# Optimization experiments

Hardware: AMD Instinct MI355X
Metric: run time of the kernel (lower is better)

## Reference

```python
import jax, jax.numpy as jnp
import numpy as np

N_NODES = 20000
N_EDGES = 320000
D_IN = 512
D_OUT = 512


def setup_inputs() -> dict:
    key = jax.random.key(0)
    k1, k2, k3, k4, k5, k6 = jax.random.split(key, 6)
    stdv = 1.0 / np.sqrt(D_OUT)
    return {
        "h": jax.random.normal(k1, (N_NODES, D_IN), dtype=jnp.float32),
        "weight": jax.random.uniform(k2, (D_IN, D_OUT), dtype=jnp.float32, minval=-stdv, maxval=stdv),
        "bias": jax.random.uniform(k3, (D_OUT,), dtype=jnp.float32, minval=-stdv, maxval=stdv),
        # GCN symmetric normalization term per node (deg^{-1/2}); strictly positive
        "norm": jax.random.uniform(k4, (N_NODES, 1), dtype=jnp.float32, minval=0.05, maxval=1.0),
        "src": jax.random.randint(k5, (N_EDGES,), 0, N_NODES, dtype=jnp.int32),
        "dst": jax.random.randint(k6, (N_EDGES,), 0, N_NODES, dtype=jnp.int32),
    }


def reference(h, weight, bias, norm, src, dst):
    # dropout p=0 -> identity (eval mode)
    # pre-normalize after dense projection: [N, d_out]
    hw = norm * jnp.matmul(h, weight)
    # update_all(copy_u, sum): gather source features, scatter-sum into dst
    msg = hw[src]  # [E, d_out]
    agg = jax.ops.segment_sum(msg, dst, num_segments=N_NODES)  # [N, d_out]
    out = agg * norm + bias
    return jax.nn.relu(out)
```

## Files before the change

### kernel.cpp

```cpp
#include <hip/hip_runtime.h>

#define M_NODES 20000
#define N_EDGES_C 320000
#define DIM 512

typedef __attribute__((ext_vector_type(4))) float f32x4;
typedef __attribute__((ext_vector_type(4))) __bf16 bf16x4;
typedef __attribute__((ext_vector_type(8))) __bf16 bf16x8;

__device__ __forceinline__ void async16(__bf16* lds, const __bf16* g) {
  __builtin_amdgcn_global_load_lds(
      (const __attribute__((address_space(1))) void*)g,
      (__attribute__((address_space(3))) void*)lds, 16, 0, 0);
}

__global__ __launch_bounds__(256) void zero_k(int4* __restrict__ counts4) {
  const int i = blockIdx.x * 256 + threadIdx.x;
  if (i < M_NODES / 4) counts4[i] = int4{0, 0, 0, 0};
}

__global__ __launch_bounds__(256) void pre_k(const float* __restrict__ h,
                                             const float* __restrict__ w,
                                             const float* __restrict__ norm,
                                             const int* __restrict__ dst,
                                             __bf16* __restrict__ hb,
                                             __bf16* __restrict__ wT,
                                             int* __restrict__ counts) {
  const int bid = blockIdx.x;
  const int tid = threadIdx.x;
  const int gtid = bid * 256 + tid;
  const int gsz = gridDim.x * 256;

  for (int i = gtid; i < M_NODES * DIM / 4; i += gsz) {
    const int elem = i * 4;
    const float s = norm[elem >> 9];
    f32x4 v = *(const f32x4*)&h[elem];
    bf16x4 o;
    o.x = (__bf16)(v.x * s);
    o.y = (__bf16)(v.y * s);
    o.z = (__bf16)(v.z * s);
    o.w = (__bf16)(v.w * s);
    *(bf16x4*)&hb[elem] = o;
  }

  if (bid < 256) {
    __shared__ float tile[32][33];
    const int bx = (bid & 15) * 32, by = (bid >> 4) * 32;
    const int tx = tid & 31, ty8 = tid >> 5;
#pragma unroll
    for (int st = 0; st < 4; ++st) {
      const int r = ty8 + st * 8;
      tile[r][tx] = w[(by + r) * DIM + bx + tx];
    }
    __syncthreads();
#pragma unroll
    for (int st = 0; st < 4; ++st) {
      const int r = ty8 + st * 8;
      wT[(bx + r) * DIM + by + tx] = (__bf16)tile[tx][r];
    }
  }

  for (int e = gtid; e < N_EDGES_C; e += gsz) atomicAdd(&counts[dst[e]], 1);
}

__global__ __launch_bounds__(256) void scan_k(int* __restrict__ counts,
                                              int* __restrict__ offsets) {
  __shared__ int wsum2[4];
  const int tid = threadIdx.x;
  const int lane = tid & 63, wid = tid >> 6;
  const int base = tid * 80;
  int s = 0;
  if (tid < 250) {
#pragma unroll
    for (int i = 0; i < 80; i += 4) {
      int4 c = *(const int4*)&counts[base + i];
      s += c.x + c.y + c.z + c.w;
    }
  }
  int x = s;
#pragma unroll
  for (int off = 1; off < 64; off <<= 1) {
    int t = __shfl_up(x, off, 64);
    if (lane >= off) x += t;
  }
  if (lane == 63) wsum2[wid] = x;
  __syncthreads();
  int wbase = 0;
  for (int wI = 0; wI < wid; ++wI) wbase += wsum2[wI];
  int run = wbase + x - s;
  if (tid < 250) {
#pragma unroll
    for (int i = 0; i < 80; i += 4) {
      int4 c = *(const int4*)&counts[base + i];
      int4 o;
      o.x = run;
      o.y = run + c.x;
      o.z = o.y + c.y;
      o.w = o.z + c.z;
      *(int4*)&offsets[base + i] = o;
      *(int4*)&counts[base + i] = o;
      run = o.w + c.w;
    }
  }
  if (tid == 0) {
    int tot = 0;
#pragma unroll
    for (int wI = 0; wI < 4; ++wI) tot += wsum2[wI];
    offsets[M_NODES] = tot;
  }
}

__global__ __launch_bounds__(256) void fill_k(const int* __restrict__ src,
                                              const int* __restrict__ dst,
                                              int* __restrict__ cursor,
                                              int* __restrict__ esrc) {
  int e = blockIdx.x * 256 + threadIdx.x;
  if (e < N_EDGES_C) {
    int p = atomicAdd(&cursor[dst[e]], 1);
    esrc[p] = src[e];
  }
}

__global__ __launch_bounds__(256) void aggregate_k(const __bf16* __restrict__ hb,
                                                   const int* __restrict__ offs,
                                                   const int* __restrict__ esrc,
                                                   __bf16* __restrict__ aggb) {
  const int panel = blockIdx.x & 7;
  const int nb = blockIdx.x >> 3;
  const int wv = threadIdx.x >> 6;
  const int lane = threadIdx.x & 63;
  const int slot = lane >> 3;
  const int cg = lane & 7;
  const int node = nb * 32 + wv * 8 + slot;

  const int beg = offs[node], end = offs[node + 1];
  const size_t pbase = (size_t)panel * 64 + cg * 8;

  float a[8] = {};
  int j = beg;
  while (j + 8 <= end) {
    const int idx = esrc[j + cg];
    int sid[8];
#pragma unroll
    for (int g = 0; g < 8; ++g) sid[g] = __shfl(idx, (lane & 56) + g, 64);
    bf16x8 v[8];
#pragma unroll
    for (int g = 0; g < 8; ++g)
      v[g] = *(const bf16x8*)&hb[(size_t)sid[g] * DIM + pbase];
#pragma unroll
    for (int g = 0; g < 8; ++g)
#pragma unroll
      for (int q = 0; q < 8; ++q) a[q] += (float)v[g][q];
    j += 8;
  }
  for (; j < end; ++j) {
    const int s0 = esrc[j];
    bf16x8 v0 = *(const bf16x8*)&hb[(size_t)s0 * DIM + pbase];
#pragma unroll
    for (int q = 0; q < 8; ++q) a[q] += (float)v0[q];
  }
  bf16x8 o;
#pragma unroll
  for (int q = 0; q < 8; ++q) o[q] = (__bf16)a[q];
  *(bf16x8*)&aggb[(size_t)node * DIM + pbase] = o;
}

__global__ __launch_bounds__(256, 2) void gemm_k(const __bf16* __restrict__ A,
                                                 const __bf16* __restrict__ B,
                                                 const float* __restrict__ bias,
                                                 const float* __restrict__ norm,
                                                 float* __restrict__ C) {
  __shared__ __bf16 As[2][64 * 64];
  __shared__ __bf16 Bs[2][128 * 64];
  const int tid = threadIdx.x;
  const int lane = tid & 63;
  const int wv = tid >> 6;
  const int wr = wv >> 1, wc = wv & 1;
  const int m0 = blockIdx.x * 64;
  const int n0 = blockIdx.y * 128;

  f32x4 acc[2][4] = {};

  const int srow = tid >> 3;
  const int scol = ((tid & 7) ^ (srow & 7)) * 8;

  auto stage = [&](int buf, int kt) {
    const int kb = kt * 64 + scol;
#pragma unroll
    for (int jj = 0; jj < 2; ++jj) {
      const int lrow = jj * 32 + srow;
      int arow = m0 + lrow;
      arow = arow < M_NODES ? arow : (M_NODES - 1);
      async16(&As[buf][lrow * 64 + (tid & 7) * 8], A + (size_t)arow * DIM + kb);
    }
#pragma unroll
    for (int jj = 0; jj < 4; ++jj) {
      const int lrow = jj * 32 + srow;
      async16(&Bs[buf][lrow * 64 + (tid & 7) * 8], B + (size_t)(n0 + lrow) * DIM + kb);
    }
  };

  stage(0, 0);
  __syncthreads();

  int cur = 0;
  for (int kt = 0; kt < DIM / 64; ++kt) {
    if (kt + 1 < DIM / 64) stage(cur ^ 1, kt + 1);
#pragma unroll
    for (int kk = 0; kk < 64; kk += 32) {
      const int c = (kk >> 3) + (lane >> 4);
      bf16x8 af[2], bfr[4];
#pragma unroll
      for (int m = 0; m < 2; ++m) {
        const int r = wr * 32 + m * 16 + (lane & 15);
        af[m] = *(const bf16x8*)&As[cur][r * 64 + ((c ^ (r & 7)) * 8)];
      }
#pragma unroll
      for (int n = 0; n < 4; ++n) {
        const int r = wc * 64 + n * 16 + (lane & 15);
        bfr[n] = *(const bf16x8*)&Bs[cur][r * 64 + ((c ^ (r & 7)) * 8)];
      }
#pragma unroll
      for (int m = 0; m < 2; ++m)
#pragma unroll
        for (int n = 0; n < 4; ++n)
          acc[m][n] = __builtin_amdgcn_mfma_f32_16x16x32_bf16(af[m], bfr[n], acc[m][n], 0, 0, 0);
    }
    __syncthreads();
    cur ^= 1;
  }

#pragma unroll
  for (int m = 0; m < 2; ++m) {
    const int rbase = m0 + wr * 32 + m * 16 + (lane >> 4) * 4;
#pragma unroll
    for (int r = 0; r < 4; ++r) {
      const int row = rbase + r;
      if (row < M_NODES) {
        const float nv = norm[row];
#pragma unroll
        for (int n = 0; n < 4; ++n) {
          const int col = n0 + wc * 64 + n * 16 + (lane & 15);
          float v = acc[m][n][r] * nv + bias[col];
          C[(size_t)row * DIM + col] = v > 0.f ? v : 0.f;
        }
      }
    }
  }
}

#define HB_OFF   0UL
#define AGG_OFF  20480000UL
#define WT_OFF   40960000UL
#define CNT_OFF  41484288UL
#define OFS_OFF  41564288UL
#define ESRC_OFF 41644544UL
#define WS_NEEDED 42924544UL

extern "C" void kernel_launch(void* const* d_in, const int* in_sizes, int n_in,
                              void* d_out, int out_size, void* d_ws, size_t ws_size,
                              hipStream_t stream) {
  const float* h    = (const float*)d_in[0];
  const float* w    = (const float*)d_in[1];
  const float* bias = (const float*)d_in[2];
  const float* norm = (const float*)d_in[3];
  const int*   src  = (const int*)d_in[4];
  const int*   dst  = (const int*)d_in[5];
  float* out = (float*)d_out;

  if (ws_size < WS_NEEDED) return;

  char* ws = (char*)d_ws;
  __bf16* hb      = (__bf16*)(ws + HB_OFF);
  __bf16* aggb    = (__bf16*)(ws + AGG_OFF);
  __bf16* wT      = (__bf16*)(ws + WT_OFF);
  int*    counts  = (int*)(ws + CNT_OFF);
  int*    offsets = (int*)(ws + OFS_OFF);
  int*    esrc    = (int*)(ws + ESRC_OFF);

  zero_k<<<20, 256, 0, stream>>>((int4*)counts);
  pre_k<<<2048, 256, 0, stream>>>(h, w, norm, dst, hb, wT, counts);
  scan_k<<<1, 256, 0, stream>>>(counts, offsets);
  fill_k<<<1250, 256, 0, stream>>>(src, dst, counts, esrc);
  aggregate_k<<<5000, 256, 0, stream>>>(hb, offsets, esrc, aggb);
  gemm_k<<<dim3(313, 4), 256, 0, stream>>>(aggb, wT, bias, norm, out);
}
```

Before: 119.7 us.

## Fold scan into pre kernel via last-block detection; triple-buffer GEMM pipeline

The separate single-block scan launch is removed. The last block to finish pre_k, detected with an atomic arrival counter, now performs the prefix scan, which saves one kernel launch and its gap. The GEMM moves from double to triple-buffered LDS staging, with explicit vmcnt waits and one barrier per k-step, so loads run two stages ahead. This raises LDS use per block, which may reduce occupancy, and it relies on correct fence and atomic ordering for the counts.

```diff
diff --git a/kernel.cpp b/kernel.cpp
--- a/kernel.cpp
+++ b/kernel.cpp
@@ -14,9 +14,11 @@
       (__attribute__((address_space(3))) void*)lds, 16, 0, 0);
 }
 
-__global__ __launch_bounds__(256) void zero_k(int4* __restrict__ counts4) {
+__global__ __launch_bounds__(256) void zero_k(int4* __restrict__ counts4,
+                                              int* __restrict__ arrive) {
   const int i = blockIdx.x * 256 + threadIdx.x;
   if (i < M_NODES / 4) counts4[i] = int4{0, 0, 0, 0};
+  if (i == 0) *arrive = 0;
 }
 
 __global__ __launch_bounds__(256) void pre_k(const float* __restrict__ h,
@@ -25,7 +27,9 @@
                                              const int* __restrict__ dst,
                                              __bf16* __restrict__ hb,
                                              __bf16* __restrict__ wT,
-                                             int* __restrict__ counts) {
+                                             int* __restrict__ counts,
+                                             int* __restrict__ offsets,
+                                             int* __restrict__ arrive) {
   const int bid = blockIdx.x;
   const int tid = threadIdx.x;
   const int gtid = bid * 256 + tid;
@@ -61,52 +65,53 @@
   }
 
   for (int e = gtid; e < N_EDGES_C; e += gsz) atomicAdd(&counts[dst[e]], 1);
-}
-
-__global__ __launch_bounds__(256) void scan_k(int* __restrict__ counts,
-                                              int* __restrict__ offsets) {
+
   __shared__ int wsum2[4];
-  const int tid = threadIdx.x;
-  const int lane = tid & 63, wid = tid >> 6;
-  const int base = tid * 80;
-  int s = 0;
-  if (tid < 250) {
-#pragma unroll
-    for (int i = 0; i < 80; i += 4) {
-      int4 c = *(const int4*)&counts[base + i];
-      s += c.x + c.y + c.z + c.w;
-    }
-  }
-  int x = s;
-#pragma unroll
-  for (int off = 1; off < 64; off <<= 1) {
-    int t = __shfl_up(x, off, 64);
-    if (lane >= off) x += t;
-  }
-  if (lane == 63) wsum2[wid] = x;
+  __shared__ int s_last;
+  __threadfence();
   __syncthreads();
-  int wbase = 0;
-  for (int wI = 0; wI < wid; ++wI) wbase += wsum2[wI];
-  int run = wbase + x - s;
-  if (tid < 250) {
-#pragma unroll
-    for (int i = 0; i < 80; i += 4) {
-      int4 c = *(const int4*)&counts[base + i];
-      int4 o;
-      o.x = run;
-      o.y = run + c.x;
-      o.z = o.y + c.y;
-      o.w = o.z + c.z;
-      *(int4*)&offsets[base + i] = o;
-      *(int4*)&counts[base + i] = o;
-      run = o.w + c.w;
-    }
-  }
   if (tid == 0) {
-    int tot = 0;
-#pragma unroll
-    for (int wI = 0; wI < 4; ++wI) tot += wsum2[wI];
-    offsets[M_NODES] = tot;
+    int prev = atomicAdd(arrive, 1);
+    s_last = (prev == (int)gridDim.x - 1) ? 1 : 0;
+  }
+  __syncthreads();
+  if (s_last) {
+    const int lane = tid & 63, wid = tid >> 6;
+    const int base = tid * 80;
+    int s = 0;
+    if (tid < 250) {
+#pragma unroll
+      for (int i = 0; i < 80; ++i)
+        s += __hip_atomic_load(&counts[base + i], __ATOMIC_RELAXED,
+                               __HIP_MEMORY_SCOPE_AGENT);
+    }
+    int x = s;
+#pragma unroll
+    for (int off = 1; off < 64; off <<= 1) {
+      int t = __shfl_up(x, off, 64);
+      if (lane >= off) x += t;
+    }
+    if (lane == 63) wsum2[wid] = x;
+    __syncthreads();
+    int wbase = 0;
+    for (int wI = 0; wI < wid; ++wI) wbase += wsum2[wI];
+    int run = wbase + x - s;
+    if (tid < 250) {
+#pragma unroll
+      for (int i = 0; i < 80; ++i) {
+        const int c = __hip_atomic_load(&counts[base + i], __ATOMIC_RELAXED,
+                                        __HIP_MEMORY_SCOPE_AGENT);
+        offsets[base + i] = run;
+        counts[base + i] = run;
+        run += c;
+      }
+    }
+    if (tid == 0) {
+      int tot = 0;
+#pragma unroll
+      for (int wI = 0; wI < 4; ++wI) tot += wsum2[wI];
+      offsets[M_NODES] = tot;
+    }
   }
 }
 
@@ -170,8 +175,8 @@
                                                  const float* __restrict__ bias,
                                                  const float* __restrict__ norm,
                                                  float* __restrict__ C) {
-  __shared__ __bf16 As[2][64 * 64];
-  __shared__ __bf16 Bs[2][128 * 64];
+  __shared__ __bf16 As[3][64 * 64];
+  __shared__ __bf16 Bs[3][128 * 64];
   const int tid = threadIdx.x;
   const int lane = tid & 63;
   const int wv = tid >> 6;
@@ -183,6 +188,7 @@
 
   const int srow = tid >> 3;
   const int scol = ((tid & 7) ^ (srow & 7)) * 8;
+  const int ldst = (tid & 7) * 8;
 
   auto stage = [&](int buf, int kt) {
     const int kb = kt * 64 + scol;
@@ -191,21 +197,32 @@
       const int lrow = jj * 32 + srow;
       int arow = m0 + lrow;
       arow = arow < M_NODES ? arow : (M_NODES - 1);
-      async16(&As[buf][lrow * 64 + (tid & 7) * 8], A + (size_t)arow * DIM + kb);
+      async16(&As[buf][lrow * 64 + ldst], A + (size_t)arow * DIM + kb);
     }
 #pragma unroll
     for (int jj = 0; jj < 4; ++jj) {
       const int lrow = jj * 32 + srow;
-      async16(&Bs[buf][lrow * 64 + (tid & 7) * 8], B + (size_t)(n0 + lrow) * DIM + kb);
+      async16(&Bs[buf][lrow * 64 + ldst], B + (size_t)(n0 + lrow) * DIM + kb);
     }
   };
 
   stage(0, 0);
-  __syncthreads();
-
-  int cur = 0;
+  stage(1, 1);
+
+  int cb = 0;
   for (int kt = 0; kt < DIM / 64; ++kt) {
-    if (kt + 1 < DIM / 64) stage(cur ^ 1, kt + 1);
+    if (kt < DIM / 64 - 1)
+      asm volatile("s_waitcnt vmcnt(6)" ::: "memory");
+    else
+      asm volatile("s_waitcnt vmcnt(0)" ::: "memory");
+    __builtin_amdgcn_s_barrier();
+    asm volatile("" ::: "memory");
+
+    if (kt + 2 < DIM / 64) {
+      int sb = cb + 2; if (sb >= 3) sb -= 3;
+      stage(sb, kt + 2);
+    }
+
 #pragma unroll
     for (int kk = 0; kk < 64; kk += 32) {
       const int c = (kk >> 3) + (lane >> 4);
@@ -213,12 +230,12 @@
 #pragma unroll
       for (int m = 0; m < 2; ++m) {
         const int r = wr * 32 + m * 16 + (lane & 15);
-        af[m] = *(const bf16x8*)&As[cur][r * 64 + ((c ^ (r & 7)) * 8)];
+        af[m] = *(const bf16x8*)&As[cb][r * 64 + ((c ^ (r & 7)) * 8)];
       }
 #pragma unroll
       for (int n = 0; n < 4; ++n) {
         const int r = wc * 64 + n * 16 + (lane & 15);
-        bfr[n] = *(const bf16x8*)&Bs[cur][r * 64 + ((c ^ (r & 7)) * 8)];
+        bfr[n] = *(const bf16x8*)&Bs[cb][r * 64 + ((c ^ (r & 7)) * 8)];
       }
 #pragma unroll
       for (int m = 0; m < 2; ++m)
@@ -226,8 +243,7 @@
         for (int n = 0; n < 4; ++n)
           acc[m][n] = __builtin_amdgcn_mfma_f32_16x16x32_bf16(af[m], bfr[n], acc[m][n], 0, 0, 0);
     }
-    __syncthreads();
-    cur ^= 1;
+    cb = (cb == 2) ? 0 : cb + 1;
   }
 
 #pragma unroll
@@ -255,7 +271,8 @@
 #define CNT_OFF  41484288UL
 #define OFS_OFF  41564288UL
 #define ESRC_OFF 41644544UL
-#define WS_NEEDED 42924544UL
+#define ARR_OFF  42924544UL
+#define WS_NEEDED 42924560UL
 
 extern "C" void kernel_launch(void* const* d_in, const int* in_sizes, int n_in,
                               void* d_out, int out_size, void* d_ws, size_t ws_size,
@@ -277,10 +294,10 @@
   int*    counts  = (int*)(ws + CNT_OFF);
   int*    offsets = (int*)(ws + OFS_OFF);
   int*    esrc    = (int*)(ws + ESRC_OFF);
-
-  zero_k<<<20, 256, 0, stream>>>((int4*)counts);
-  pre_k<<<2048, 256, 0, stream>>>(h, w, norm, dst, hb, wT, counts);
-  scan_k<<<1, 256, 0, stream>>>(counts, offsets);
+  int*    arrive  = (int*)(ws + ARR_OFF);
+
+  zero_k<<<20, 256, 0, stream>>>((int4*)counts, arrive);
+  pre_k<<<2048, 256, 0, stream>>>(h, w, norm, dst, hb, wT, counts, offsets, arrive);
   fill_k<<<1250, 256, 0, stream>>>(src, dst, counts, esrc);
   aggregate_k<<<5000, 256, 0, stream>>>(hb, offsets, esrc, aggb);
   gemm_k<<<dim3(313, 4), 256, 0, stream>>>(aggb, wT, bias, norm, out);
```

Result: slower. 290.2 us (+142.4%).

## Drop LDS staging in GEMM and load MFMA fragments directly from global memory

Applied to the files above, without the earlier changes.

The bf16 GEMM no longer uses a double-buffered LDS pipeline fed by async global-to-LDS copies. Each wave now loads its A and B MFMA fragments straight from global memory on every 32-wide k step. This removes LDS traffic, barriers and the LDS occupancy limit, and drops the launch-bounds occupancy hint. The cost is that nothing is shared between waves: each B fragment is fetched by two waves and each A fragment by two waves, with no explicit prefetch to overlap load latency with MFMA work.

```diff
diff --git a/kernel.cpp b/kernel.cpp
--- a/kernel.cpp
+++ b/kernel.cpp
@@ -7,12 +7,6 @@
 typedef __attribute__((ext_vector_type(4))) float f32x4;
 typedef __attribute__((ext_vector_type(4))) __bf16 bf16x4;
 typedef __attribute__((ext_vector_type(8))) __bf16 bf16x8;
-
-__device__ __forceinline__ void async16(__bf16* lds, const __bf16* g) {
-  __builtin_amdgcn_global_load_lds(
-      (const __attribute__((address_space(1))) void*)g,
-      (__attribute__((address_space(3))) void*)lds, 16, 0, 0);
-}
 
 __global__ __launch_bounds__(256) void zero_k(int4* __restrict__ counts4) {
   const int i = blockIdx.x * 256 + threadIdx.x;
@@ -165,13 +159,11 @@
   *(bf16x8*)&aggb[(size_t)node * DIM + pbase] = o;
 }
 
-__global__ __launch_bounds__(256, 2) void gemm_k(const __bf16* __restrict__ A,
-                                                 const __bf16* __restrict__ B,
-                                                 const float* __restrict__ bias,
-                                                 const float* __restrict__ norm,
-                                                 float* __restrict__ C) {
-  __shared__ __bf16 As[2][64 * 64];
-  __shared__ __bf16 Bs[2][128 * 64];
+__global__ __launch_bounds__(256) void gemm_k(const __bf16* __restrict__ A,
+                                              const __bf16* __restrict__ B,
+                                              const float* __restrict__ bias,
+                                              const float* __restrict__ norm,
+                                              float* __restrict__ C) {
   const int tid = threadIdx.x;
   const int lane = tid & 63;
   const int wv = tid >> 6;
@@ -181,53 +173,28 @@
 
   f32x4 acc[2][4] = {};
 
-  const int srow = tid >> 3;
-  const int scol = ((tid & 7) ^ (srow & 7)) * 8;
-
-  auto stage = [&](int buf, int kt) {
-    const int kb = kt * 64 + scol;
-#pragma unroll
-    for (int jj = 0; jj < 2; ++jj) {
-      const int lrow = jj * 32 + srow;
-      int arow = m0 + lrow;
-      arow = arow < M_NODES ? arow : (M_NODES - 1);
-      async16(&As[buf][lrow * 64 + (tid & 7) * 8], A + (size_t)arow * DIM + kb);
-    }
-#pragma unroll
-    for (int jj = 0; jj < 4; ++jj) {
-      const int lrow = jj * 32 + srow;
-      async16(&Bs[buf][lrow * 64 + (tid & 7) * 8], B + (size_t)(n0 + lrow) * DIM + kb);
-    }
-  };
-
-  stage(0, 0);
-  __syncthreads();
-
-  int cur = 0;
-  for (int kt = 0; kt < DIM / 64; ++kt) {
-    if (kt + 1 < DIM / 64) stage(cur ^ 1, kt + 1);
-#pragma unroll
-    for (int kk = 0; kk < 64; kk += 32) {
-      const int c = (kk >> 3) + (lane >> 4);
-      bf16x8 af[2], bfr[4];
-#pragma unroll
-      for (int m = 0; m < 2; ++m) {
-        const int r = wr * 32 + m * 16 + (lane & 15);
-        af[m] = *(const bf16x8*)&As[cur][r * 64 + ((c ^ (r & 7)) * 8)];
-      }
-#pragma unroll
-      for (int n = 0; n < 4; ++n) {
-        const int r = wc * 64 + n * 16 + (lane & 15);
-        bfr[n] = *(const bf16x8*)&Bs[cur][r * 64 + ((c ^ (r & 7)) * 8)];
-      }
-#pragma unroll
-      for (int m = 0; m < 2; ++m)
-#pragma unroll
-        for (int n = 0; n < 4; ++n)
-          acc[m][n] = __builtin_amdgcn_mfma_f32_16x16x32_bf16(af[m], bfr[n], acc[m][n], 0, 0, 0);
-    }
-    __syncthreads();
-    cur ^= 1;
+  const int lr = lane & 15;
+  const int kc = (lane >> 4) * 8;
+  int arow0 = m0 + wr * 32 + lr;
+  int arow1 = arow0 + 16;
+  arow0 = arow0 < M_NODES ? arow0 : (M_NODES - 1);
+  arow1 = arow1 < M_NODES ? arow1 : (M_NODES - 1);
+  const __bf16* __restrict__ a0 = A + (size_t)arow0 * DIM + kc;
+  const __bf16* __restrict__ a1 = A + (size_t)arow1 * DIM + kc;
+  const __bf16* __restrict__ b0 = B + (size_t)(n0 + wc * 64 + lr) * DIM + kc;
+
+  for (int kt = 0; kt < DIM; kt += 32) {
+    bf16x8 af[2], bfr[4];
+    af[0] = *(const bf16x8*)(a0 + kt);
+    af[1] = *(const bf16x8*)(a1 + kt);
+#pragma unroll
+    for (int n = 0; n < 4; ++n)
+      bfr[n] = *(const bf16x8*)(b0 + (size_t)n * 16 * DIM + kt);
+#pragma unroll
+    for (int m = 0; m < 2; ++m)
+#pragma unroll
+      for (int n = 0; n < 4; ++n)
+        acc[m][n] = __builtin_amdgcn_mfma_f32_16x16x32_bf16(af[m], bfr[n], acc[m][n], 0, 0, 0);
   }
 
 #pragma unroll
```

Result: slower. 153.0 us (+27.8%).

## Widen GEMM tile to full 512-column output per block with K=32 stages

Applied to the files above, without the earlier changes.

The final GEMM now uses 512-thread blocks, each computing a 64x512 output tile, so every A tile is loaded once instead of four times across column blocks. The K step drops from 64 to 32 with a new 4-way XOR swizzle to fit the larger B tile in LDS, and each wave holds 2x8 accumulators. In exchange there are twice as many k-iterations and barriers, more registers per wave, and only 313 blocks, which may underfill the GPU's compute units.

```diff
diff --git a/kernel.cpp b/kernel.cpp
--- a/kernel.cpp
+++ b/kernel.cpp
@@ -165,38 +165,37 @@
   *(bf16x8*)&aggb[(size_t)node * DIM + pbase] = o;
 }
 
-__global__ __launch_bounds__(256, 2) void gemm_k(const __bf16* __restrict__ A,
+__global__ __launch_bounds__(512, 2) void gemm_k(const __bf16* __restrict__ A,
                                                  const __bf16* __restrict__ B,
                                                  const float* __restrict__ bias,
                                                  const float* __restrict__ norm,
                                                  float* __restrict__ C) {
-  __shared__ __bf16 As[2][64 * 64];
-  __shared__ __bf16 Bs[2][128 * 64];
+  __shared__ __bf16 As[2][64 * 32];
+  __shared__ __bf16 Bs[2][512 * 32];
   const int tid = threadIdx.x;
   const int lane = tid & 63;
   const int wv = tid >> 6;
-  const int wr = wv >> 1, wc = wv & 1;
+  const int wm = wv >> 2;
+  const int wn = wv & 3;
   const int m0 = blockIdx.x * 64;
-  const int n0 = blockIdx.y * 128;
-
-  f32x4 acc[2][4] = {};
-
-  const int srow = tid >> 3;
-  const int scol = ((tid & 7) ^ (srow & 7)) * 8;
+
+  f32x4 acc[2][8] = {};
 
   auto stage = [&](int buf, int kt) {
-    const int kb = kt * 64 + scol;
-#pragma unroll
-    for (int jj = 0; jj < 2; ++jj) {
-      const int lrow = jj * 32 + srow;
-      int arow = m0 + lrow;
+    const int kb = kt * 32;
+    const int p = tid & 3;
+    if (tid < 256) {
+      const int row = tid >> 2;
+      const int g = p ^ ((row >> 2) & 3);
+      int arow = m0 + row;
       arow = arow < M_NODES ? arow : (M_NODES - 1);
-      async16(&As[buf][lrow * 64 + (tid & 7) * 8], A + (size_t)arow * DIM + kb);
-    }
-#pragma unroll
-    for (int jj = 0; jj < 4; ++jj) {
-      const int lrow = jj * 32 + srow;
-      async16(&Bs[buf][lrow * 64 + (tid & 7) * 8], B + (size_t)(n0 + lrow) * DIM + kb);
+      async16(&As[buf][row * 32 + p * 8], A + (size_t)arow * DIM + kb + g * 8);
+    }
+#pragma unroll
+    for (int j = 0; j < 4; ++j) {
+      const int row = (tid >> 2) + j * 128;
+      const int g = p ^ ((row >> 2) & 3);
+      async16(&Bs[buf][row * 32 + p * 8], B + (size_t)row * DIM + kb + g * 8);
     }
   };
 
@@ -204,43 +203,40 @@
   __syncthreads();
 
   int cur = 0;
-  for (int kt = 0; kt < DIM / 64; ++kt) {
-    if (kt + 1 < DIM / 64) stage(cur ^ 1, kt + 1);
-#pragma unroll
-    for (int kk = 0; kk < 64; kk += 32) {
-      const int c = (kk >> 3) + (lane >> 4);
-      bf16x8 af[2], bfr[4];
-#pragma unroll
-      for (int m = 0; m < 2; ++m) {
-        const int r = wr * 32 + m * 16 + (lane & 15);
-        af[m] = *(const bf16x8*)&As[cur][r * 64 + ((c ^ (r & 7)) * 8)];
-      }
-#pragma unroll
-      for (int n = 0; n < 4; ++n) {
-        const int r = wc * 64 + n * 16 + (lane & 15);
-        bfr[n] = *(const bf16x8*)&Bs[cur][r * 64 + ((c ^ (r & 7)) * 8)];
-      }
-#pragma unroll
-      for (int m = 0; m < 2; ++m)
-#pragma unroll
-        for (int n = 0; n < 4; ++n)
-          acc[m][n] = __builtin_amdgcn_mfma_f32_16x16x32_bf16(af[m], bfr[n], acc[m][n], 0, 0, 0);
-    }
+  for (int kt = 0; kt < DIM / 32; ++kt) {
+    if (kt + 1 < DIM / 32) stage(cur ^ 1, kt + 1);
+    const int c = lane >> 4;
+    bf16x8 af[2], bfr[8];
+#pragma unroll
+    for (int m = 0; m < 2; ++m) {
+      const int r = wm * 32 + m * 16 + (lane & 15);
+      af[m] = *(const bf16x8*)&As[cur][r * 32 + ((c ^ ((r >> 2) & 3)) * 8)];
+    }
+#pragma unroll
+    for (int n = 0; n < 8; ++n) {
+      const int r = wn * 128 + n * 16 + (lane & 15);
+      bfr[n] = *(const bf16x8*)&Bs[cur][r * 32 + ((c ^ ((r >> 2) & 3)) * 8)];
+    }
+#pragma unroll
+    for (int m = 0; m < 2; ++m)
+#pragma unroll
+      for (int n = 0; n < 8; ++n)
+        acc[m][n] = __builtin_amdgcn_mfma_f32_16x16x32_bf16(af[m], bfr[n], acc[m][n], 0, 0, 0);
     __syncthreads();
     cur ^= 1;
   }
 
 #pragma unroll
   for (int m = 0; m < 2; ++m) {
-    const int rbase = m0 + wr * 32 + m * 16 + (lane >> 4) * 4;
+    const int rbase = m0 + wm * 32 + m * 16 + (lane >> 4) * 4;
 #pragma unroll
     for (int r = 0; r < 4; ++r) {
       const int row = rbase + r;
       if (row < M_NODES) {
         const float nv = norm[row];
 #pragma unroll
-        for (int n = 0; n < 4; ++n) {
-          const int col = n0 + wc * 64 + n * 16 + (lane & 15);
+        for (int n = 0; n < 8; ++n) {
+          const int col = wn * 128 + n * 16 + (lane & 15);
           float v = acc[m][n][r] * nv + bias[col];
           C[(size_t)row * DIM + col] = v > 0.f ? v : 0.f;
         }
@@ -283,5 +279,5 @@
   scan_k<<<1, 256, 0, stream>>>(counts, offsets);
   fill_k<<<1250, 256, 0, stream>>>(src, dst, counts, esrc);
   aggregate_k<<<5000, 256, 0, stream>>>(hb, offsets, esrc, aggb);
-  gemm_k<<<dim3(313, 4), 256, 0, stream>>>(aggb, wT, bias, norm, out);
-}
+  gemm_k<<<313, 512, 0, stream>>>(aggb, wT, bias, norm, out);
+}
```

Result: slower. 133.5 us (+11.5%).
